# Performance work log

Hardware: AMD Instinct MI355X
Metric: run time of the kernel (lower is better)

Reference implementation:

```python
import jax, jax.numpy as jnp
import numpy as np

POOL_D, POOL_H, POOL_W = 4, 7, 7
SPATIAL_SCALE = 0.25
SAMPLING_RATIO = 2


def setup_inputs() -> dict:
    key = jax.random.key(0)
    k1, k2, k3, k4 = jax.random.split(key, 4)
    N, C, D, H, W = 2, 128, 32, 64, 64
    features = jax.random.normal(k1, (N, C, D, H, W), dtype=jnp.float32)
    R = 256
    inv = 1.0 / SPATIAL_SCALE  # rois live in image coords; features at stride 4
    batch = jax.random.randint(k2, (R,), 0, N).astype(jnp.float32)
    dims = jnp.array([D, H, W], dtype=jnp.float32)
    starts = jax.random.uniform(k3, (R, 3)) * dims * inv * 0.6
    sizes = (0.1 + 0.3 * jax.random.uniform(k4, (R, 3))) * dims * inv
    z1, y1, x1 = starts[:, 0], starts[:, 1], starts[:, 2]
    z2, y2, x2 = z1 + sizes[:, 0], y1 + sizes[:, 1], x1 + sizes[:, 2]
    # roi layout: (batch_idx, x1, y1, z1, x2, y2, z2)
    rois = jnp.stack([batch, x1, y1, z1, x2, y2, z2], axis=1).astype(jnp.float32)
    return {"features": features, "rois": rois}


def _axis(coords, size):
    # classic RoIAlign border handling: outside [-1, size] -> 0 contribution
    valid = (coords >= -1.0) & (coords <= float(size))
    c = jnp.clip(coords, 0.0, float(size) - 1.0)
    lo = jnp.floor(c)
    hi = jnp.minimum(lo + 1.0, float(size) - 1.0)
    w = c - lo  # weight of the hi corner
    return lo.astype(jnp.int32), hi.astype(jnp.int32), w, valid


def roi_align_3d(features, rois):
    N, C, D, H, W = features.shape
    R = rois.shape[0]
    sr = SAMPLING_RATIO
    b = rois[:, 0].astype(jnp.int32)
    x1 = rois[:, 1] * SPATIAL_SCALE
    y1 = rois[:, 2] * SPATIAL_SCALE
    z1 = rois[:, 3] * SPATIAL_SCALE
    x2 = rois[:, 4] * SPATIAL_SCALE
    y2 = rois[:, 5] * SPATIAL_SCALE
    z2 = rois[:, 6] * SPATIAL_SCALE
    rd = jnp.maximum(z2 - z1, 1.0)
    rh = jnp.maximum(y2 - y1, 1.0)
    rw = jnp.maximum(x2 - x1, 1.0)

    def sample_coords(start, extent, P):
        # sampling_ratio sample centers per output bin -> [R, P*sr]
        t = (jnp.arange(P * sr, dtype=jnp.float32) + 0.5) / sr
        return start[:, None] + t[None, :] * (extent / P)[:, None]

    zs = sample_coords(z1, rd, POOL_D)  # [R, SD]
    ys = sample_coords(y1, rh, POOL_H)  # [R, SH]
    xs = sample_coords(x1, rw, POOL_W)  # [R, SW]
    zlo, zhi, wz, vz = _axis(zs, D)
    ylo, yhi, wy, vy = _axis(ys, H)
    xlo, xhi, wx, vx = _axis(xs, W)

    B = b[:, None, None, None]
    Z = lambda a: a[:, :, None, None]
    Y = lambda a: a[:, None, :, None]
    X = lambda a: a[:, None, None, :]

    def g(zi, yi, xi):
        # gather -> [R, SD, SH, SW, C]
        return features[B, :, Z(zi), Y(yi), X(xi)]

    wz1, wy1, wx1 = Z(wz)[..., None], Y(wy)[..., None], X(wx)[..., None]
    wz0, wy0, wx0 = 1.0 - wz1, 1.0 - wy1, 1.0 - wx1
    val = (g(zlo, ylo, xlo) * (wz0 * wy0 * wx0)
           + g(zlo, ylo, xhi) * (wz0 * wy0 * wx1)
           + g(zlo, yhi, xlo) * (wz0 * wy1 * wx0)
           + g(zlo, yhi, xhi) * (wz0 * wy1 * wx1)
           + g(zhi, ylo, xlo) * (wz1 * wy0 * wx0)
           + g(zhi, ylo, xhi) * (wz1 * wy0 * wx1)
           + g(zhi, yhi, xlo) * (wz1 * wy1 * wx0)
           + g(zhi, yhi, xhi) * (wz1 * wy1 * wx1))
    valid = (Z(vz) & Y(vy) & X(vx))[..., None]
    val = jnp.where(valid, val, 0.0)
    # average the sr^3 samples per bin
    val = val.reshape(R, POOL_D, sr, POOL_H, sr, POOL_W, sr, C)
    out = val.mean(axis=(2, 4, 6))  # [R, PD, PH, PW, C]
    return jnp.transpose(out, (0, 4, 1, 2, 3))  # [R, C, PD, PH, PW]


def reference(features, rois):
    return roi_align_3d(features, rois)
```

## Files before the change

kernel.cpp:

```cpp
#include <hip/hip_runtime.h>

constexpr int C_  = 128;
constexpr int D_  = 32;
constexpr int H_  = 64;
constexpr int W_  = 64;
constexpr int PD = 4;
constexpr int PH = 7;
constexpr int PW = 7;
constexpr int SR = 2;
constexpr float SCALE = 0.25f;
constexpr int S_ = D_ * H_ * W_;
constexpr int BINS_PER_ROI = PD * PH * PW;
constexpr int SLAB = PH * PW;

typedef float vf4 __attribute__((ext_vector_type(4)));

__device__ __forceinline__ void axis2(float start, float extent, int P, int p,
                                      int size, int lo[2], int hi[2],
                                      float w[2], bool v[2]) {
    float bin = extent / (float)P;
#pragma unroll
    for (int u = 0; u < 2; ++u) {
        float t = ((float)(p * SR + u) + 0.5f) / (float)SR;
        float coord = start + t * bin;
        v[u] = (coord >= -1.0f) && (coord <= (float)size);
        float cc = fminf(fmaxf(coord, 0.0f), (float)size - 1.0f);
        float fl = floorf(cc);
        lo[u] = (int)fl;
        hi[u] = min(lo[u] + 1, size - 1);
        w[u] = cc - fl;
    }
}

__device__ __forceinline__ unsigned int f2bf(float f) {
    unsigned int u = __float_as_uint(f);
    u += 0x7fffu + ((u >> 16) & 1u);
    return u >> 16;
}

__device__ __forceinline__ float4 bf4(uint2 v) {
    float4 f;
    f.x = __uint_as_float(v.x << 16);
    f.y = __uint_as_float(v.x & 0xffff0000u);
    f.z = __uint_as_float(v.y << 16);
    f.w = __uint_as_float(v.y & 0xffff0000u);
    return f;
}

__global__ __launch_bounds__(512) void transpose_bf16(
    const float* __restrict__ in, unsigned int* __restrict__ outp) {
    __shared__ unsigned int tileu[256][64];
    const int n  = blockIdx.y;
    const int s0 = blockIdx.x * 256;
    const int t  = threadIdx.x;

    const float* src = in + (size_t)n * C_ * S_;
    unsigned int* dst = outp + (size_t)n * (C_ / 2) * S_;

    {
        const int sl  = t & 63;
        const int cp0 = t >> 6;
#pragma unroll
        for (int p = 0; p < 8; ++p) {
            const int cp = cp0 + 8 * p;
            const int c = cp * 2;
            const vf4 a = __builtin_nontemporal_load(
                (const vf4*)&src[(size_t)c * S_ + (s0 + 4 * sl)]);
            const vf4 b = __builtin_nontemporal_load(
                (const vf4*)&src[(size_t)(c + 1) * S_ + (s0 + 4 * sl)]);
            const int col = cp ^ (sl & 31);
            tileu[4 * sl + 0][col] = f2bf(a.x) | (f2bf(b.x) << 16);
            tileu[4 * sl + 1][col] = f2bf(a.y) | (f2bf(b.y) << 16);
            tileu[4 * sl + 2][col] = f2bf(a.z) | (f2bf(b.z) << 16);
            tileu[4 * sl + 3][col] = f2bf(a.w) | (f2bf(b.w) << 16);
        }
    }
    __syncthreads();
    {
        const int cp2   = (t & 31) * 2;
        const int rbase = t >> 5;
#pragma unroll
        for (int it = 0; it < 16; ++it) {
            const int s = rbase + 16 * it;
            const int w = (s >> 2) & 31;
            uint2 v;
            v.x = tileu[s][cp2 ^ w];
            v.y = tileu[s][(cp2 + 1) ^ w];
            *(uint2*)&dst[(size_t)(s0 + s) * (C_ / 2) + cp2] = v;
        }
    }
}

__global__ __launch_bounds__(512) void roi_align_slab(
    const unsigned short* __restrict__ ft,
    const float* __restrict__ rois,
    float* __restrict__ out,
    int R) {
    __shared__ __align__(16) float tile[SLAB][132];

    int r, pd;
    if ((R & 7) == 0) {
        const int xcd = blockIdx.x & 7;
        const int q = blockIdx.x >> 3;
        pd = q & 3;
        r = ((q >> 2) << 3) + xcd;
    } else {
        r = blockIdx.x >> 2;
        pd = blockIdx.x & 3;
    }

    const int t = threadIdx.x;
    const int grp = t >> 5;
    const int c4 = (t & 31) * 4;

    const float* roi = rois + (size_t)r * 7;
    const int b = (int)roi[0];
    const float x1 = roi[1] * SCALE, y1 = roi[2] * SCALE, z1 = roi[3] * SCALE;
    const float x2 = roi[4] * SCALE, y2 = roi[5] * SCALE, z2 = roi[6] * SCALE;
    const float rd = fmaxf(z2 - z1, 1.0f);
    const float rh = fmaxf(y2 - y1, 1.0f);
    const float rw = fmaxf(x2 - x1, 1.0f);

    int zlo[2], zhi[2];
    float wz[2];
    bool vz[2];
    axis2(z1, rd, PD, pd, D_, zlo, zhi, wz, vz);

#pragma unroll 1
    for (int k = 0; k < 4; ++k) {
        const int slot = grp + 16 * k;
        if (slot < SLAB) {
            const int ph = slot / PW;
            const int pw = slot - ph * PW;

            int ylo[2], yhi[2], xlo[2], xhi[2];
            float wy[2], wx[2];
            bool vy[2], vx[2];
            axis2(y1, rh, PH, ph, H_, ylo, yhi, wy, vy);
            axis2(x1, rw, PW, pw, W_, xlo, xhi, wx, vx);

            float4 acc = make_float4(0.f, 0.f, 0.f, 0.f);
#pragma unroll
            for (int i = 0; i < 2; ++i) {
                if (!vz[i]) continue;
                const float wz1 = wz[i], wz0 = 1.0f - wz1;
#pragma unroll
                for (int j = 0; j < 2; ++j) {
                    if (!vy[j]) continue;
                    const float wy1 = wy[j], wy0 = 1.0f - wy1;
                    const size_t r00 =
                        (((size_t)b * D_ + zlo[i]) * H_ + ylo[j]) * W_;
                    const size_t r10 =
                        (((size_t)b * D_ + zhi[i]) * H_ + ylo[j]) * W_;
                    const size_t r01 =
                        (((size_t)b * D_ + zlo[i]) * H_ + yhi[j]) * W_;
                    const size_t r11 =
                        (((size_t)b * D_ + zhi[i]) * H_ + yhi[j]) * W_;
#pragma unroll
                    for (int kk = 0; kk < 2; ++kk) {
                        if (!vx[kk]) continue;
                        const float wx1 = wx[kk], wx0 = 1.0f - wx1;
                        const size_t xl = xlo[kk], xh = xhi[kk];
                        const float4 f000 =
                            bf4(*(const uint2*)&ft[(r00 + xl) * C_ + c4]);
                        const float4 f001 =
                            bf4(*(const uint2*)&ft[(r00 + xh) * C_ + c4]);
                        const float4 f010 =
                            bf4(*(const uint2*)&ft[(r01 + xl) * C_ + c4]);
                        const float4 f011 =
                            bf4(*(const uint2*)&ft[(r01 + xh) * C_ + c4]);
                        const float4 f100 =
                            bf4(*(const uint2*)&ft[(r10 + xl) * C_ + c4]);
                        const float4 f101 =
                            bf4(*(const uint2*)&ft[(r10 + xh) * C_ + c4]);
                        const float4 f110 =
                            bf4(*(const uint2*)&ft[(r11 + xl) * C_ + c4]);
                        const float4 f111 =
                            bf4(*(const uint2*)&ft[(r11 + xh) * C_ + c4]);
                        const float w000 = wz0 * wy0 * wx0,
                                    w001 = wz0 * wy0 * wx1;
                        const float w010 = wz0 * wy1 * wx0,
                                    w011 = wz0 * wy1 * wx1;
                        const float w100 = wz1 * wy0 * wx0,
                                    w101 = wz1 * wy0 * wx1;
                        const float w110 = wz1 * wy1 * wx0,
                                    w111 = wz1 * wy1 * wx1;
                        acc.x += w000 * f000.x + w001 * f001.x +
                                 w010 * f010.x + w011 * f011.x +
                                 w100 * f100.x + w101 * f101.x +
                                 w110 * f110.x + w111 * f111.x;
                        acc.y += w000 * f000.y + w001 * f001.y +
                                 w010 * f010.y + w011 * f011.y +
                                 w100 * f100.y + w101 * f101.y +
                                 w110 * f110.y + w111 * f111.y;
                        acc.z += w000 * f000.z + w001 * f001.z +
                                 w010 * f010.z + w011 * f011.z +
                                 w100 * f100.z + w101 * f101.z +
                                 w110 * f110.z + w111 * f111.z;
                        acc.w += w000 * f000.w + w001 * f001.w +
                                 w010 * f010.w + w011 * f011.w +
                                 w100 * f100.w + w101 * f101.w +
                                 w110 * f110.w + w111 * f111.w;
                    }
                }
            }
            const float s = 1.0f / (SR * SR * SR);
            acc.x *= s; acc.y *= s; acc.z *= s; acc.w *= s;
            *(float4*)&tile[slot][c4] = acc;
        }
    }

    __syncthreads();

    const size_t obase = (size_t)r * C_ * BINS_PER_ROI + (size_t)pd * SLAB;
#pragma unroll 1
    for (int idx = t; idx < C_ * SLAB; idx += 512) {
        const int c = idx / SLAB;
        const int o = idx - c * SLAB;
        __builtin_nontemporal_store(tile[o][c],
                                    &out[obase + (size_t)c * BINS_PER_ROI + o]);
    }
}

__global__ void roi_align_direct(const float* __restrict__ feat,
                                 const float* __restrict__ rois,
                                 float* __restrict__ out, int total) {
    const int tid = blockIdx.x * blockDim.x + threadIdx.x;
    if (tid >= total) return;
    int t = tid;
    const int pw = t % PW; t /= PW;
    const int ph = t % PH; t /= PH;
    const int pd = t % PD; t /= PD;
    const int c = t % C_;  t /= C_;
    const int r = t;

    const float* roi = rois + (size_t)r * 7;
    const int b = (int)roi[0];
    const float x1 = roi[1] * SCALE, y1 = roi[2] * SCALE, z1 = roi[3] * SCALE;
    const float x2 = roi[4] * SCALE, y2 = roi[5] * SCALE, z2 = roi[6] * SCALE;
    const float rd = fmaxf(z2 - z1, 1.0f);
    const float rh = fmaxf(y2 - y1, 1.0f);
    const float rw = fmaxf(x2 - x1, 1.0f);

    int zlo[2], zhi[2], ylo[2], yhi[2], xlo[2], xhi[2];
    float wz[2], wy[2], wx[2];
    bool vz[2], vy[2], vx[2];
    axis2(z1, rd, PD, pd, D_, zlo, zhi, wz, vz);
    axis2(y1, rh, PH, ph, H_, ylo, yhi, wy, vy);
    axis2(x1, rw, PW, pw, W_, xlo, xhi, wx, vx);

    const float* fc = feat + ((size_t)b * C_ + c) * S_;
    float acc = 0.0f;
#pragma unroll
    for (int i = 0; i < 2; ++i) {
        if (!vz[i]) continue;
#pragma unroll
        for (int j = 0; j < 2; ++j) {
            if (!vy[j]) continue;
            const size_t r00 = ((size_t)zlo[i] * H_ + ylo[j]) * W_;
            const size_t r10 = ((size_t)zhi[i] * H_ + ylo[j]) * W_;
            const size_t r01 = ((size_t)zlo[i] * H_ + yhi[j]) * W_;
            const size_t r11 = ((size_t)zhi[i] * H_ + yhi[j]) * W_;
            const float wz1 = wz[i], wz0 = 1.0f - wz1;
            const float wy1 = wy[j], wy0 = 1.0f - wy1;
#pragma unroll
            for (int k = 0; k < 2; ++k) {
                if (!vx[k]) continue;
                const float wx1 = wx[k], wx0 = 1.0f - wx1;
                acc += wz0 * (wy0 * (wx0 * fc[r00 + xlo[k]] + wx1 * fc[r00 + xhi[k]]) +
                              wy1 * (wx0 * fc[r01 + xlo[k]] + wx1 * fc[r01 + xhi[k]])) +
                       wz1 * (wy0 * (wx0 * fc[r10 + xlo[k]] + wx1 * fc[r10 + xhi[k]]) +
                              wy1 * (wx0 * fc[r11 + xlo[k]] + wx1 * fc[r11 + xhi[k]]));
            }
        }
    }
    out[tid] = acc * (1.0f / (SR * SR * SR));
}

extern "C" void kernel_launch(void* const* d_in, const int* in_sizes, int n_in,
                              void* d_out, int out_size, void* d_ws,
                              size_t ws_size, hipStream_t stream) {
    const float* features = (const float*)d_in[0];
    const float* rois = (const float*)d_in[1];
    float* out = (float*)d_out;

    const int R = in_sizes[1] / 7;
    const int N = in_sizes[0] / (C_ * S_);
    const size_t need = (size_t)in_sizes[0] * sizeof(unsigned short);

    if (ws_size >= need) {
        unsigned short* ft = (unsigned short*)d_ws;

        dim3 tg(S_ / 256, N);
        transpose_bf16<<<tg, 512, 0, stream>>>(features, (unsigned int*)ft);

        roi_align_slab<<<R * PD, 512, 0, stream>>>(ft, rois, out, R);
    } else {
        const int total = R * C_ * BINS_PER_ROI;
        roi_align_direct<<<(total + 255) / 256, 256, 0, stream>>>(
            features, rois, out, total);
    }
}
```

Baseline: 259.1 us.

## Merge per-axis sample weights into a 4-tap window to dedupe gathers

```diff
diff --git a/kernel.cpp b/kernel.cpp
--- a/kernel.cpp
+++ b/kernel.cpp
@@ -30,6 +30,55 @@
         hi[u] = min(lo[u] + 1, size - 1);
         w[u] = cc - fl;
     }
+}
+
+struct AxisW {
+    int base;
+    float w[4];
+};
+
+__device__ __forceinline__ AxisW axis_merge(float start, float extent, int P,
+                                            int p, int size) {
+    const float bin = extent / (float)P;
+    const float t0 = ((float)(p * SR) + 0.5f) / (float)SR;
+    const float c0 = start + t0 * bin;
+    const float va = (c0 >= -1.0f && c0 <= (float)size) ? 1.0f : 0.0f;
+    const float cc0 = fminf(fmaxf(c0, 0.0f), (float)size - 1.0f);
+    const float fl0 = floorf(cc0);
+    const int lo0 = (int)fl0;
+    const int hi0 = min(lo0 + 1, size - 1);
+    const float f0 = cc0 - fl0;
+    const float a0 = (1.0f - f0) * va;
+    const float a1 = f0 * va;
+    const float t1 = ((float)(p * SR + 1) + 0.5f) / (float)SR;
+    const float c1 = start + t1 * bin;
+    const float vb = (c1 >= -1.0f && c1 <= (float)size) ? 1.0f : 0.0f;
+    const float cc1 = fminf(fmaxf(c1, 0.0f), (float)size - 1.0f);
+    const float fl1 = floorf(cc1);
+    const int lo1 = (int)fl1;
+    const int hi1 = min(lo1 + 1, size - 1);
+    const float f1 = cc1 - fl1;
+    const float b0 = (1.0f - f1) * vb;
+    const float b1 = f1 * vb;
+
+    const int dh0 = hi0 - lo0;
+    const int dl1 = lo1 - lo0;
+    const int dh1 = hi1 - lo0;
+
+    float w0 = a0, w1 = 0.f, w2 = 0.f, w3 = 0.f;
+    if (dh0 == 0) w0 += a1; else w1 += a1;
+    w0 += (dl1 == 0) ? b0 : 0.f;
+    w1 += (dl1 == 1) ? b0 : 0.f;
+    w2 += (dl1 == 2) ? b0 : 0.f;
+    w0 += (dh1 == 0) ? b1 : 0.f;
+    w1 += (dh1 == 1) ? b1 : 0.f;
+    w2 += (dh1 == 2) ? b1 : 0.f;
+    w3 += (dh1 == 3) ? b1 : 0.f;
+
+    AxisW r;
+    r.base = lo0;
+    r.w[0] = w0; r.w[1] = w1; r.w[2] = w2; r.w[3] = w3;
+    return r;
 }
 
 __device__ __forceinline__ unsigned int f2bf(float f) {
@@ -121,10 +170,11 @@
     const float rh = fmaxf(y2 - y1, 1.0f);
     const float rw = fmaxf(x2 - x1, 1.0f);
 
-    int zlo[2], zhi[2];
-    float wz[2];
-    bool vz[2];
-    axis2(z1, rd, PD, pd, D_, zlo, zhi, wz, vz);
+    AxisW az = axis_merge(z1, rd, PD, pd, D_);
+    {
+        const float s = 1.0f / (SR * SR * SR);
+        az.w[0] *= s; az.w[1] *= s; az.w[2] *= s; az.w[3] *= s;
+    }
 
 #pragma unroll 1
     for (int k = 0; k < 4; ++k) {
@@ -133,79 +183,38 @@
             const int ph = slot / PW;
             const int pw = slot - ph * PW;
 
-            int ylo[2], yhi[2], xlo[2], xhi[2];
-            float wy[2], wx[2];
-            bool vy[2], vx[2];
-            axis2(y1, rh, PH, ph, H_, ylo, yhi, wy, vy);
-            axis2(x1, rw, PW, pw, W_, xlo, xhi, wx, vx);
+            const AxisW ay = axis_merge(y1, rh, PH, ph, H_);
+            const AxisW ax = axis_merge(x1, rw, PW, pw, W_);
 
             float4 acc = make_float4(0.f, 0.f, 0.f, 0.f);
-#pragma unroll
-            for (int i = 0; i < 2; ++i) {
-                if (!vz[i]) continue;
-                const float wz1 = wz[i], wz0 = 1.0f - wz1;
-#pragma unroll
-                for (int j = 0; j < 2; ++j) {
-                    if (!vy[j]) continue;
-                    const float wy1 = wy[j], wy0 = 1.0f - wy1;
-                    const size_t r00 =
-                        (((size_t)b * D_ + zlo[i]) * H_ + ylo[j]) * W_;
-                    const size_t r10 =
-                        (((size_t)b * D_ + zhi[i]) * H_ + ylo[j]) * W_;
-                    const size_t r01 =
-                        (((size_t)b * D_ + zlo[i]) * H_ + yhi[j]) * W_;
-                    const size_t r11 =
-                        (((size_t)b * D_ + zhi[i]) * H_ + yhi[j]) * W_;
-#pragma unroll
-                    for (int kk = 0; kk < 2; ++kk) {
-                        if (!vx[kk]) continue;
-                        const float wx1 = wx[kk], wx0 = 1.0f - wx1;
-                        const size_t xl = xlo[kk], xh = xhi[kk];
-                        const float4 f000 =
-                            bf4(*(const uint2*)&ft[(r00 + xl) * C_ + c4]);
-                        const float4 f001 =
-                            bf4(*(const uint2*)&ft[(r00 + xh) * C_ + c4]);
-                        const float4 f010 =
-                            bf4(*(const uint2*)&ft[(r01 + xl) * C_ + c4]);
-                        const float4 f011 =
-                            bf4(*(const uint2*)&ft[(r01 + xh) * C_ + c4]);
-                        const float4 f100 =
-                            bf4(*(const uint2*)&ft[(r10 + xl) * C_ + c4]);
-                        const float4 f101 =
-                            bf4(*(const uint2*)&ft[(r10 + xh) * C_ + c4]);
-                        const float4 f110 =
-                            bf4(*(const uint2*)&ft[(r11 + xl) * C_ + c4]);
-                        const float4 f111 =
-                            bf4(*(const uint2*)&ft[(r11 + xh) * C_ + c4]);
-                        const float w000 = wz0 * wy0 * wx0,
-                                    w001 = wz0 * wy0 * wx1;
-                        const float w010 = wz0 * wy1 * wx0,
-                                    w011 = wz0 * wy1 * wx1;
-                        const float w100 = wz1 * wy0 * wx0,
-                                    w101 = wz1 * wy0 * wx1;
-                        const float w110 = wz1 * wy1 * wx0,
-                                    w111 = wz1 * wy1 * wx1;
-                        acc.x += w000 * f000.x + w001 * f001.x +
-                                 w010 * f010.x + w011 * f011.x +
-                                 w100 * f100.x + w101 * f101.x +
-                                 w110 * f110.x + w111 * f111.x;
-                        acc.y += w000 * f000.y + w001 * f001.y +
-                                 w010 * f010.y + w011 * f011.y +
-                                 w100 * f100.y + w101 * f101.y +
-                                 w110 * f110.y + w111 * f111.y;
-                        acc.z += w000 * f000.z + w001 * f001.z +
-                                 w010 * f010.z + w011 * f011.z +
-                                 w100 * f100.z + w101 * f101.z +
-                                 w110 * f110.z + w111 * f111.z;
-                        acc.w += w000 * f000.w + w001 * f001.w +
-                                 w010 * f010.w + w011 * f011.w +
-                                 w100 * f100.w + w101 * f101.w +
-                                 w110 * f110.w + w111 * f111.w;
+            const unsigned bz = (unsigned)b * D_ + (unsigned)az.base;
+#pragma unroll
+            for (int iz = 0; iz < 4; ++iz) {
+                const float wzv = az.w[iz];
+                if (wzv == 0.0f) continue;
+                const unsigned rz = (bz + iz) * H_ + (unsigned)ay.base;
+#pragma unroll
+                for (int iy = 0; iy < 4; ++iy) {
+                    const float wyv = ay.w[iy];
+                    if (wyv == 0.0f) continue;
+                    const float wzy = wzv * wyv;
+                    const unsigned rowoff =
+                        ((rz + iy) * W_ + (unsigned)ax.base) * C_ + c4;
+                    const unsigned short* rowp = ft + rowoff;
+#pragma unroll
+                    for (int ix = 0; ix < 4; ++ix) {
+                        const float wxv = ax.w[ix];
+                        if (wxv == 0.0f) continue;
+                        const float4 f =
+                            bf4(*(const uint2*)(rowp + ix * C_));
+                        const float w = wzy * wxv;
+                        acc.x += w * f.x;
+                        acc.y += w * f.y;
+                        acc.z += w * f.z;
+                        acc.w += w * f.w;
                     }
                 }
             }
-            const float s = 1.0f / (SR * SR * SR);
-            acc.x *= s; acc.y *= s; acc.z *= s; acc.w *= s;
             *(float4*)&tile[slot][c4] = acc;
         }
     }
```

Result: slower. 278.6 us (+7.5%).
